# Performance work log

Measured on AMD Instinct MI355X. Metric: run time of the kernel, lower is better.

The kernel has to match this reference:

```python
import jax, jax.numpy as jnp
import numpy as np

L = 4          # stack_size
H = 1024       # hidden_size
N = 16         # num_heads
D = H // N     # size_per_head = 64
F = 4096       # filter_size
B = 2
QLEN = 512
MLEN = 512
CLEN = QLEN + MLEN    # 1024
RLEN = CLEN + QLEN    # 1536
NEG_INF = -1e30
LN_EPS = 1e-12


def setup_inputs() -> dict:
    key = jax.random.key(0)
    ks = jax.random.split(key, 24)
    s = 0.02
    inp = {
        'content_stream': jax.random.normal(ks[0], (B, QLEN, H), jnp.float32),
        'content_mask': jnp.zeros((B, 1, QLEN, CLEN), jnp.float32),
        'position_encoding': jax.random.normal(ks[1], (B, RLEN, H), jnp.float32),
        'segment_matrix': jax.random.randint(ks[2], (B, QLEN, CLEN), 0, 2).astype(bool),
        'mems': jax.random.normal(ks[3], (L, B, MLEN, H), jnp.float32),
        # per-layer attention projection weights [L, H, N, D]
        'w_q': jax.random.normal(ks[4], (L, H, N, D), jnp.float32) * s,
        'w_k': jax.random.normal(ks[5], (L, H, N, D), jnp.float32) * s,
        'w_v': jax.random.normal(ks[6], (L, H, N, D), jnp.float32) * s,
        'w_r': jax.random.normal(ks[7], (L, H, N, D), jnp.float32) * s,
        'w_o': jax.random.normal(ks[8], (L, H, N, D), jnp.float32) * s,
        # FFN
        'ffn_w1': jax.random.normal(ks[9], (L, H, F), jnp.float32) * s,
        'ffn_b1': jnp.zeros((L, F), jnp.float32),
        'ffn_w2': jax.random.normal(ks[10], (L, F, H), jnp.float32) * s,
        'ffn_b2': jnp.zeros((L, H), jnp.float32),
        # LayerNorms (post-attn and post-ffn)
        'ln1_gamma': jnp.ones((L, H), jnp.float32),
        'ln1_beta': jnp.zeros((L, H), jnp.float32),
        'ln2_gamma': jnp.ones((L, H), jnp.float32),
        'ln2_beta': jnp.zeros((L, H), jnp.float32),
        # tied biases [N, D] and per-layer segment encoding [L, 2, N, D]
        'content_bias': jax.random.normal(ks[11], (N, D), jnp.float32) * H ** -0.5,
        'position_bias': jax.random.normal(ks[12], (N, D), jnp.float32) * H ** -0.5,
        'segment_bias': jax.random.normal(ks[13], (N, D), jnp.float32) * H ** -0.5,
        'segment_encoding': jax.random.normal(ks[14], (L, 2, N, D), jnp.float32) * H ** -0.5,
    }
    return inp


def _rel_shift(x, klen):
    # x: [b, n, q, r] -> rel-shifted and sliced to [b, n, q, klen]
    b, n, q, r = x.shape
    x = x.reshape(b, n, r, q)[:, :, 1:, :]
    x = x.reshape(b, n, q, r - 1)[:, :, :, :klen]
    return x


def _layernorm(x, gamma, beta):
    mu = jnp.mean(x, axis=-1, keepdims=True)
    var = jnp.mean(jnp.square(x - mu), axis=-1, keepdims=True)
    return (x - mu) * jax.lax.rsqrt(var + LN_EPS) * gamma + beta


def _forward(content_stream, content_mask, position_encoding, segment_matrix,
             mems, w_q, w_k, w_v, w_r, w_o, ffn_w1, ffn_b1, ffn_w2, ffn_b2,
             ln1_gamma, ln1_beta, ln2_gamma, ln2_beta,
             content_bias, position_bias, segment_bias, segment_encoding):
    x = content_stream
    seg = segment_matrix[:, None, :, :]  # [b,1,q,c]
    for l in range(L):
        context = jnp.concatenate([mems[l], x], axis=1)  # [b,c,h]
        q = jnp.einsum('bih,hnd->bind', x, w_q[l])
        k = jnp.einsum('bjh,hnd->bjnd', context, w_k[l])
        v = jnp.einsum('bjh,hnd->bjnd', context, w_v[l])
        r = jnp.einsum('brh,hnd->brnd', position_encoding, w_r[l])
        # content term
        ac = jnp.einsum('bind,bjnd->bnij', q + content_bias, k)
        # position term with rel-shift trick
        bd = jnp.einsum('bind,brnd->bnir', q + position_bias, r)
        bd = _rel_shift(bd, CLEN)
        # segment term: s in {0: different, 1: same-ish binary indicator}
        ef2 = jnp.einsum('bind,snd->bnis', q + segment_bias, segment_encoding[l])
        ef = jnp.where(seg, ef2[..., 1:2], ef2[..., 0:1])  # [b,n,q,c]
        scores = (ac + bd + ef) * (D ** -0.5)
        scores = scores + content_mask * NEG_INF  # mask==1 -> blocked
        probs = jax.nn.softmax(scores, axis=-1)
        attn = jnp.einsum('bnij,bjnd->bind', probs, v)
        attn_out = jnp.einsum('bind,hnd->bih', attn, w_o[l])
        # post-LN residual blocks (dropout is identity at inference)
        y = _layernorm(attn_out + x, ln1_gamma[l], ln1_beta[l])
        ffn = jnp.maximum(y @ ffn_w1[l] + ffn_b1[l], 0.0) @ ffn_w2[l] + ffn_b2[l]
        x = _layernorm(ffn + y, ln2_gamma[l], ln2_beta[l])
    return x


def reference(content_stream, content_mask, position_encoding, segment_matrix,
              mems, w_q, w_k, w_v, w_r, w_o, ffn_w1, ffn_b1, ffn_w2, ffn_b2,
              ln1_gamma, ln1_beta, ln2_gamma, ln2_beta,
              content_bias, position_bias, segment_bias, segment_encoding):
    return _forward(content_stream, content_mask, position_encoding,
                    segment_matrix, mems, w_q, w_k, w_v, w_r, w_o,
                    ffn_w1, ffn_b1, ffn_w2, ffn_b2,
                    ln1_gamma, ln1_beta, ln2_gamma, ln2_beta,
                    content_bias, position_bias, segment_bias, segment_encoding)
```

## Files before the change

### kernel.cpp

```cpp
#include <hip/hip_runtime.h>
#include <hip/hip_bf16.h>


#define BQ 2
#define QL 512
#define ML 512
#define CL 1024
#define RL 1536
#define HD 1024
#define NH 16
#define DH 64
#define FF 4096
#define NLAYER 4

typedef const float* FP;
typedef const __hip_bfloat16* BP;
typedef unsigned short u16;
typedef __attribute__((ext_vector_type(8))) __bf16 bf16x8;
typedef __attribute__((ext_vector_type(4))) float f32x4;

static __device__ __forceinline__ float b2f(__hip_bfloat16 x) { return __bfloat162float(x); }
static __device__ __forceinline__ u16 f2u(float f) {
    union { __hip_bfloat16 h; u16 u; } c; c.h = __float2bfloat16(f); return c.u;
}
static __device__ __forceinline__ float u2f(u16 u) {
    union { float f; unsigned int i; } c; c.i = ((unsigned int)u) << 16; return c.f;
}

static __device__ __forceinline__ void gll16(const u16* g, u16* l) {
    __builtin_amdgcn_global_load_lds(
        (__attribute__((address_space(1))) void*)(u16*)g,
        (__attribute__((address_space(3))) void*)l, 16, 0, 0);
}

__global__ void sniff_kernel(const unsigned int* __restrict__ ln1_gamma,
                             const unsigned char* __restrict__ seg,
                             int* __restrict__ flags) {
    if (threadIdx.x == 0) {
        flags[0] = (ln1_gamma[0] == 0x3F800000u) ? 1 : 0;
        int int32ok = 1;
        for (int i = 0; i < 256; ++i)
            if ((i & 3) != 0 && seg[i] != 0) { int32ok = 0; break; }
        flags[1] = int32ok;
    }
}

__global__ void canon_kernel(FP inf, BP inb, u16* __restrict__ out,
                             int n, const int* __restrict__ flags) {
    int i = blockIdx.x * 256 + threadIdx.x;
    if (i >= n) return;
    out[i] = flags[0] ? f2u(inf[i]) : ((const u16*)inb)[i];
}

__global__ void out_write_kernel(const u16* __restrict__ in, void* __restrict__ out,
                                 int n, const int* __restrict__ flags) {
    int i = blockIdx.x * 256 + threadIdx.x;
    if (i >= n) return;
    if (flags[0]) ((float*)out)[i] = u2f(in[i]);
    else          ((u16*)out)[i] = in[i];
}

__global__ void segmask_pack_kernel(const void* __restrict__ seg,
                                    FP maskf, BP maskb,
                                    unsigned char* __restrict__ segp,
                                    u16* __restrict__ maskS,
                                    const int* __restrict__ flags) {
    int i = blockIdx.x * 256 + threadIdx.x;
    if (i >= BQ * QL * CL) return;
    int sv = flags[1] ? ((const int*)seg)[i] : (int)((const signed char*)seg)[i];
    segp[i] = sv ? 1 : 0;
    float mk = flags[0] ? maskf[i] : b2f(maskb[i]);
    maskS[i] = f2u(mk * -1e30f);
}

__global__ __launch_bounds__(256) void transpose_kernel(
    FP inf, BP inb, u16* __restrict__ out, int R, int Cc,
    const int* __restrict__ flags) {
    __shared__ float t[32][33];
    const int tid = threadIdx.x;
    const int c0 = blockIdx.x * 32, r0 = blockIdx.y * 32;
    const int tc = tid & 31, tr = tid >> 5;
    const int f32 = flags[0];
    #pragma unroll
    for (int p = 0; p < 4; ++p) {
        int r = r0 + p * 8 + tr;
        size_t gi = (size_t)r * Cc + c0 + tc;
        t[p * 8 + tr][tc] = f32 ? inf[gi] : b2f(inb[gi]);
    }
    __syncthreads();
    #pragma unroll
    for (int p = 0; p < 4; ++p) {
        int c = c0 + p * 8 + tr;
        out[(size_t)c * R + r0 + tc] = f2u(t[tc][p * 8 + tr]);
    }
}

__global__ __launch_bounds__(256) void vtrans_kernel(
    const u16* __restrict__ Vb, u16* __restrict__ VT) {
    __shared__ u16 t[32][33];
    const int tid = threadIdx.x;
    const int j0 = blockIdx.x * 32, d0 = blockIdx.y * 32, bn = blockIdx.z;
    const int b = bn >> 4, n = bn & 15;
    const int tc = tid & 31, tr = tid >> 5;
    #pragma unroll
    for (int p = 0; p < 4; ++p) {
        int j = j0 + p * 8 + tr;
        t[p * 8 + tr][tc] = Vb[((size_t)(b * CL + j) * NH + n) * DH + d0 + tc];
    }
    __syncthreads();
    #pragma unroll
    for (int p = 0; p < 4; ++p) {
        int d = d0 + p * 8 + tr;
        VT[((size_t)bn * DH + d) * CL + j0 + tc] = t[tc][p * 8 + tr];
    }
}

__global__ void build_ctx_kernel(FP memf, BP memb, const u16* __restrict__ X,
                                 u16* __restrict__ CTX, const int* __restrict__ flags) {
    int i = blockIdx.x * 256 + threadIdx.x;
    int h = i % HD;
    int r = (i / HD) % CL;
    int b = i / (HD * CL);
    if (r < ML) {
        size_t mi = ((size_t)(b * ML + r)) * HD + h;
        CTX[i] = flags[0] ? f2u(memf[mi]) : ((const u16*)memb)[mi];
    } else {
        CTX[i] = X[((size_t)(b * QL + (r - ML))) * HD + h];
    }
}

__device__ __forceinline__ void gemm128_core(
    const u16* __restrict__ A, int lda, const u16* __restrict__ Bt, int ldb,
    int K, int tid, u16* sA, u16* sB, f32x4 (&acc)[4][4])
{
    const int lane = tid & 63, w = tid >> 6;
    const int wm = (w & 1) * 64, wn = (w >> 1) * 64;
    const int lr = lane & 15, quad = lane >> 4;
    const int srow = lane >> 2;
    const int sch = (lane & 3) * 8;

    for (int k0 = 0; k0 < K; k0 += 32) {
        #pragma unroll
        for (int j = 0; j < 2; ++j) {
            int rb = w * 32 + j * 16;
            gll16(&A[(size_t)(rb + srow) * lda + k0 + sch], &sA[rb * 32 + lane * 8]);
            gll16(&Bt[(size_t)(rb + srow) * ldb + k0 + sch], &sB[rb * 32 + lane * 8]);
        }
        __syncthreads();
        bf16x8 af[4], bf[4];
        #pragma unroll
        for (int mi = 0; mi < 4; ++mi)
            af[mi] = *(const bf16x8*)&sA[(wm + mi * 16 + lr) * 32 + quad * 8];
        #pragma unroll
        for (int ni = 0; ni < 4; ++ni)
            bf[ni] = *(const bf16x8*)&sB[(wn + ni * 16 + lr) * 32 + quad * 8];
        #pragma unroll
        for (int mi = 0; mi < 4; ++mi)
            #pragma unroll
            for (int ni = 0; ni < 4; ++ni)
                acc[mi][ni] = __builtin_amdgcn_mfma_f32_16x16x32_bf16(
                    af[mi], bf[ni], acc[mi][ni], 0, 0, 0);
        __syncthreads();
    }
}

#define ACC_INIT(acc) \
    _Pragma("unroll") for (int mi = 0; mi < 4; ++mi) \
        _Pragma("unroll") for (int ni = 0; ni < 4; ++ni) \
            acc[mi][ni] = (f32x4){0.f, 0.f, 0.f, 0.f};

__global__ __launch_bounds__(256) void proj4_gemm(
    const u16* __restrict__ X, const u16* __restrict__ CTX,
    const u16* __restrict__ PE, const u16* __restrict__ W4,
    u16* __restrict__ Qb, u16* __restrict__ Kb,
    u16* __restrict__ Vb, u16* __restrict__ Rb)
{
    __shared__ __align__(16) u16 sA[128 * 32];
    __shared__ __align__(16) u16 sB[128 * 32];
    const int tid = threadIdx.x;
    const int by = blockIdx.y;
    const u16* Abase; u16* Cbase; int seg, mb;
    if (by < 8)       { seg = 0; Abase = X;   Cbase = Qb; mb = by; }
    else if (by < 24) { seg = 1; Abase = CTX; Cbase = Kb; mb = by - 8; }
    else if (by < 40) { seg = 2; Abase = CTX; Cbase = Vb; mb = by - 24; }
    else              { seg = 3; Abase = PE;  Cbase = Rb; mb = by - 40; }
    const int m0 = mb * 128, n0 = blockIdx.x * 128;

    f32x4 acc[4][4];
    ACC_INIT(acc)
    gemm128_core(Abase + (size_t)m0 * HD, HD,
                 W4 + (size_t)seg * HD * HD + (size_t)n0 * HD, HD, HD,
                 tid, sA, sB, acc);

    const int lane = tid & 63, w = tid >> 6;
    const int wm = (w & 1) * 64, wn = (w >> 1) * 64;
    const int lr = lane & 15, quad = lane >> 4;
    #pragma unroll
    for (int ni = 0; ni < 4; ++ni) {
        int col = n0 + wn + ni * 16 + lr;
        #pragma unroll
        for (int mi = 0; mi < 4; ++mi) {
            int row = m0 + wm + mi * 16 + quad * 4;
            #pragma unroll
            for (int r = 0; r < 4; ++r)
                Cbase[(size_t)(row + r) * HD + col] = f2u(acc[mi][ni][r]);
        }
    }
}

template <bool RELU, bool HASBIAS>
__global__ __launch_bounds__(256) void mfma_gemm128(
    const u16* __restrict__ A, const u16* __restrict__ Bt,
    FP biasf, BP biasb, u16* __restrict__ C,
    int N, int K, const int* __restrict__ flags)
{
    __shared__ __align__(16) u16 sA[128 * 32];
    __shared__ __align__(16) u16 sB[128 * 32];
    const int tid = threadIdx.x;
    const int n0 = blockIdx.x * 128, m0 = blockIdx.y * 128;
    f32x4 acc[4][4];
    ACC_INIT(acc)
    gemm128_core(A + (size_t)m0 * K, K, Bt + (size_t)n0 * K, K, K,
                 tid, sA, sB, acc);

    const int lane = tid & 63, w = tid >> 6;
    const int wm = (w & 1) * 64, wn = (w >> 1) * 64;
    const int lr = lane & 15, quad = lane >> 4;
    const int f32 = flags[0];
    #pragma unroll
    for (int ni = 0; ni < 4; ++ni) {
        int col = n0 + wn + ni * 16 + lr;
        float bv = 0.f;
        if (HASBIAS) bv = f32 ? biasf[col] : b2f(biasb[col]);
        #pragma unroll
        for (int mi = 0; mi < 4; ++mi) {
            int row = m0 + wm + mi * 16 + quad * 4;
            #pragma unroll
            for (int r = 0; r < 4; ++r) {
                float v = acc[mi][ni][r];
                if (HASBIAS) v += bv;
                if (RELU) v = fmaxf(v, 0.0f);
                C[(size_t)(row + r) * N + col] = f2u(v);
            }
        }
    }
}

__global__ __launch_bounds__(256) void gemm128_splitk(
    const u16* __restrict__ A, const u16* __restrict__ Bt,
    float* __restrict__ part, int N, int Kfull, int Kc)
{
    __shared__ __align__(16) u16 sA[128 * 32];
    __shared__ __align__(16) u16 sB[128 * 32];
    const int tid = threadIdx.x;
    const int n0 = blockIdx.x * 128, m0 = blockIdx.y * 128, z = blockIdx.z;
    f32x4 acc[4][4];
    ACC_INIT(acc)
    gemm128_core(A + (size_t)m0 * Kfull + z * Kc, Kfull,
                 Bt + (size_t)n0 * Kfull + z * Kc, Kfull, Kc,
                 tid, sA, sB, acc);

    float* P = part + (size_t)z * (1024 * 1024);
    const int lane = tid & 63, w = tid >> 6;
    const int wm = (w & 1) * 64, wn = (w >> 1) * 64;
    const int lr = lane & 15, quad = lane >> 4;
    #pragma unroll
    for (int ni = 0; ni < 4; ++ni) {
        int col = n0 + wn + ni * 16 + lr;
        #pragma unroll
        for (int mi = 0; mi < 4; ++mi) {
            int row = m0 + wm + mi * 16 + quad * 4;
            #pragma unroll
            for (int r = 0; r < 4; ++r)
                P[(size_t)(row + r) * N + col] = acc[mi][ni][r];
        }
    }
}

template <bool HASBIAS>
__global__ __launch_bounds__(256) void reduce_add_ln(
    const float* __restrict__ part, FP biasf, BP biasb,
    const u16* __restrict__ resid, FP gf, BP gb, FP bef, BP beb,
    u16* __restrict__ O, const int* __restrict__ flags)
{
    const int row = blockIdx.x;
    const int tid = threadIdx.x;
    const int wid = tid >> 6, lane = tid & 63;
    __shared__ float r1[4], r2[4];
    const int f32 = flags[0];
    float v[4];
    #pragma unroll
    for (int c = 0; c < 4; ++c) {
        int h = c * 256 + tid;
        size_t idx = (size_t)row * HD + h;
        float s = part[idx] + part[idx + 1048576] + part[idx + 2097152] + part[idx + 3145728];
        if (HASBIAS) s += f32 ? biasf[h] : b2f(biasb[h]);
        v[c] = s + u2f(resid[idx]);
    }
    float s = v[0] + v[1] + v[2] + v[3];
    #pragma unroll
    for (int o = 32; o > 0; o >>= 1) s += __shfl_xor(s, o);
    if (lane == 0) r1[wid] = s;
    __syncthreads();
    float mu = (r1[0] + r1[1] + r1[2] + r1[3]) * (1.0f / HD);
    float q = 0.f;
    #pragma unroll
    for (int c = 0; c < 4; ++c) { float d = v[c] - mu; q += d * d; }
    #pragma unroll
    for (int o = 32; o > 0; o >>= 1) q += __shfl_xor(q, o);
    if (lane == 0) r2[wid] = q;
    __syncthreads();
    float var = (r2[0] + r2[1] + r2[2] + r2[3]) * (1.0f / HD);
    float inv = rsqrtf(var + 1e-12f);
    #pragma unroll
    for (int c = 0; c < 4; ++c) {
        int h = c * 256 + tid;
        float g = f32 ? gf[h] : b2f(gb[h]);
        float be = f32 ? bef[h] : b2f(beb[h]);
        O[(size_t)row * HD + h] = f2u((v[c] - mu) * inv * g + be);
    }
}

__global__ void ef2_kernel(const u16* __restrict__ Qb, FP sbf, BP sbb,
                           FP sef, BP seb, float* __restrict__ EF,
                           const int* __restrict__ flags) {
    int t = blockIdx.x * 256 + threadIdx.x;
    if (t >= BQ * NH * QL) return;
    int i = t % QL;
    int n = (t / QL) % NH;
    int b = t / (QL * NH);
    float e0 = 0.f, e1 = 0.f;
    const int f32 = flags[0];
    for (int d = 0; d < DH; ++d) {
        float sbv = f32 ? sbf[n * DH + d] : b2f(sbb[n * DH + d]);
        float s0 = f32 ? sef[(0 * NH + n) * DH + d] : b2f(seb[(0 * NH + n) * DH + d]);
        float s1 = f32 ? sef[(1 * NH + n) * DH + d] : b2f(seb[(1 * NH + n) * DH + d]);
        float qv = u2f(Qb[((size_t)(b * QL + i) * NH + n) * DH + d]) + sbv;
        e0 += qv * s0;
        e1 += qv * s1;
    }
    EF[(size_t)t * 2 + 0] = e0;
    EF[(size_t)t * 2 + 1] = e1;
}

__global__ void ckpr_kernel(const u16* __restrict__ Kb, const u16* __restrict__ Rb,
                            FP cbf, BP cbb, FP pbf, BP pbb,
                            float* __restrict__ CK, float* __restrict__ PR,
                            const int* __restrict__ flags) {
    int t = blockIdx.x * 256 + threadIdx.x;
    const int f32 = flags[0];
    if (t < 32 * CL) {
        int bn = t >> 10, j = t & (CL - 1);
        int b = bn >> 4, n = bn & 15;
        float s = 0.f;
        for (int d = 0; d < DH; ++d) {
            float c = f32 ? cbf[n * DH + d] : b2f(cbb[n * DH + d]);
            s += c * u2f(Kb[((size_t)(b * CL + j) * NH + n) * DH + d]);
        }
        CK[t] = s;
    } else {
        int t2 = t - 32 * CL;
        if (t2 >= 32 * RL) return;
        int bn = t2 / RL, rr = t2 % RL;
        int b = bn >> 4, n = bn & 15;
        float s = 0.f;
        for (int d = 0; d < DH; ++d) {
            float c = f32 ? pbf[n * DH + d] : b2f(pbb[n * DH + d]);
            s += c * u2f(Rb[((size_t)(b * RL + rr) * NH + n) * DH + d]);
        }
        PR[(size_t)bn * RL + rr] = s;
    }
}

#define FA_SP 72
#define FA_SD 84
__global__ __launch_bounds__(128) void flash_attn_kernel(
    const u16* __restrict__ Qb, const u16* __restrict__ Kb,
    const u16* __restrict__ Rb, const u16* __restrict__ VT,
    const float* __restrict__ CK, const float* __restrict__ PR,
    const float* __restrict__ EF, const unsigned char* __restrict__ segp,
    const u16* __restrict__ maskS, u16* __restrict__ AT)
{
    __shared__ __align__(16) u16 sP[2][16 * FA_SP];
    __shared__ float sD[2][16 * FA_SD];
    __shared__ float cmb[64 * 25];

    const int tid = threadIdx.x;
    const int w = tid >> 6;
    const int lane = tid & 63;
    const int lr = lane & 15, quad = lane >> 4;

    const int blin = blockIdx.x;
    const int xcd = blin & 7, slot = blin >> 3;
    const int bn = xcd + 8 * (slot >> 5);
    const int itile = slot & 31;
    const int b = bn >> 4, n = bn & 15;
    const int i0 = itile * 16;

    u16* myP = sP[w];
    float* myD = sD[w];

    const size_t qoff = ((size_t)(b * QL + i0 + lr) * NH + n) * DH + quad * 8;
    const bf16x8 q0 = *(const bf16x8*)&Qb[qoff];
    const bf16x8 q1 = *(const bf16x8*)&Qb[qoff + 32];

    float ef0[4], ef1[4];
    #pragma unroll
    for (int r = 0; r < 4; ++r) {
        size_t e = ((size_t)bn * QL + i0 + quad * 4 + r) * 2;
        ef0[r] = EF[e]; ef1[r] = EF[e + 1];
    }

    f32x4 accO[4];
    #pragma unroll
    for (int c = 0; c < 4; ++c) accO[c] = (f32x4){0.f, 0.f, 0.f, 0.f};
    float m[4], l[4];
    #pragma unroll
    for (int r = 0; r < 4; ++r) { m[r] = -1e38f; l[r] = 0.f; }

    for (int t = 0; t < 8; ++t) {
        const int j0 = (2 * t + w) * 64;
        const int base16 = 497 - i0 + j0;

        f32x4 acc[4];
        #pragma unroll
        for (int c = 0; c < 4; ++c) acc[c] = (f32x4){0.f, 0.f, 0.f, 0.f};
        #pragma unroll
        for (int ct = 0; ct < 4; ++ct) {
            const u16* kp = &Kb[((size_t)(b * CL + j0 + ct * 16 + lr) * NH + n) * DH + quad * 8];
            acc[ct] = __builtin_amdgcn_mfma_f32_16x16x32_bf16(q0, *(const bf16x8*)kp, acc[ct], 0, 0, 0);
            acc[ct] = __builtin_amdgcn_mfma_f32_16x16x32_bf16(q1, *(const bf16x8*)(kp + 32), acc[ct], 0, 0, 0);
        }
        f32x4 bd[5];
        int rrl[5];
        #pragma unroll
        for (int f = 0; f < 5; ++f) {
            bd[f] = (f32x4){0.f, 0.f, 0.f, 0.f};
            int rr = base16 + f * 16 + lr;
            rr = rr > RL - 1 ? RL - 1 : rr;
            rrl[f] = rr;
            const u16* rp = &Rb[((size_t)(b * RL + rr) * NH + n) * DH + quad * 8];
            bd[f] = __builtin_amdgcn_mfma_f32_16x16x32_bf16(q0, *(const bf16x8*)rp, bd[f], 0, 0, 0);
            bd[f] = __builtin_amdgcn_mfma_f32_16x16x32_bf16(q1, *(const bf16x8*)(rp + 32), bd[f], 0, 0, 0);
        }
        #pragma unroll
        for (int f = 0; f < 5; ++f) {
            float prv = PR[(size_t)bn * RL + rrl[f]];
            #pragma unroll
            for (int r = 0; r < 4; ++r)
                myD[(quad * 4 + r) * FA_SD + f * 16 + lr] = bd[f][r] + prv;
        }
        #pragma unroll
        for (int ct = 0; ct < 4; ++ct) {
            float ckv = CK[(size_t)bn * CL + j0 + ct * 16 + lr];
            #pragma unroll
            for (int r = 0; r < 4; ++r) {
                int ilw = quad * 4 + r;
                int p = 15 - ilw + ct * 16 + lr;
                float bdv = myD[ilw * FA_SD + p];
                size_t mi = ((size_t)(b * QL + i0 + ilw)) * CL + j0 + ct * 16 + lr;
                float efv = segp[mi] ? ef1[r] : ef0[r];
                acc[ct][r] = (acc[ct][r] + bdv + ckv + efv) * 0.125f + u2f(maskS[mi]);
            }
        }
        float a[4];
        #pragma unroll
        for (int r = 0; r < 4; ++r) {
            float tm = fmaxf(fmaxf(acc[0][r], acc[1][r]), fmaxf(acc[2][r], acc[3][r]));
            tm = fmaxf(tm, __shfl_xor(tm, 1));
            tm = fmaxf(tm, __shfl_xor(tm, 2));
            tm = fmaxf(tm, __shfl_xor(tm, 4));
            tm = fmaxf(tm, __shfl_xor(tm, 8));
            float mn = fmaxf(m[r], tm);
            a[r] = __expf(m[r] - mn);
            m[r] = mn;
        }
        float ts[4] = {0.f, 0.f, 0.f, 0.f};
        #pragma unroll
        for (int ct = 0; ct < 4; ++ct)
            #pragma unroll
            for (int r = 0; r < 4; ++r) {
                float pv = __expf(acc[ct][r] - m[r]);
                ts[r] += pv;
                myP[(quad * 4 + r) * FA_SP + ct * 16 + lr] = f2u(pv);
            }
        #pragma unroll
        for (int r = 0; r < 4; ++r) {
            float s = ts[r];
            s += __shfl_xor(s, 1);
            s += __shfl_xor(s, 2);
            s += __shfl_xor(s, 4);
            s += __shfl_xor(s, 8);
            l[r] = l[r] * a[r] + s;
            #pragma unroll
            for (int c = 0; c < 4; ++c) accO[c][r] *= a[r];
        }
        const bf16x8 pa0 = *(const bf16x8*)&myP[lr * FA_SP + quad * 8];
        const bf16x8 pa1 = *(const bf16x8*)&myP[lr * FA_SP + 32 + quad * 8];
        #pragma unroll
        for (int ct = 0; ct < 4; ++ct) {
            const u16* vp = &VT[((size_t)bn * DH + ct * 16 + lr) * CL + j0 + quad * 8];
            accO[ct] = __builtin_amdgcn_mfma_f32_16x16x32_bf16(pa0, *(const bf16x8*)vp, accO[ct], 0, 0, 0);
            accO[ct] = __builtin_amdgcn_mfma_f32_16x16x32_bf16(pa1, *(const bf16x8*)(vp + 32), accO[ct], 0, 0, 0);
        }
    }
    if (w == 1) {
        float* c = &cmb[lane * 25];
        #pragma unroll
        for (int ct = 0; ct < 4; ++ct)
            #pragma unroll
            for (int r = 0; r < 4; ++r) c[ct * 4 + r] = accO[ct][r];
        #pragma unroll
        for (int r = 0; r < 4; ++r) { c[16 + r] = m[r]; c[20 + r] = l[r]; }
    }
    __syncthreads();
    if (w == 0) {
        const float* c = &cmb[lane * 25];
        float e0[4], e1[4], inv[4];
        #pragma unroll
        for (int r = 0; r < 4; ++r) {
            float m1 = c[16 + r], l1 = c[20 + r];
            float M = fmaxf(m[r], m1);
            e0[r] = __expf(m[r] - M);
            e1[r] = __expf(m1 - M);
            inv[r] = 1.0f / (l[r] * e0[r] + l1 * e1[r]);
        }
        #pragma unroll
        for (int ct = 0; ct < 4; ++ct)
            #pragma unroll
            for (int r = 0; r < 4; ++r) {
                float o = accO[ct][r] * e0[r] + c[ct * 4 + r] * e1[r];
                AT[((size_t)(b * QL + i0 + quad * 4 + r) * NH + n) * DH + ct * 16 + lr]
                    = f2u(o * inv[r]);
            }
    }
}

extern "C" void kernel_launch(void* const* d_in, const int* in_sizes, int n_in,
                              void* d_out, int out_size, void* d_ws, size_t ws_size,
                              hipStream_t stream) {
    (void)in_sizes; (void)n_in; (void)out_size; (void)ws_size;
    const void* content_stream = d_in[0];
    const void* content_mask   = d_in[1];
    const void* pos_enc        = d_in[2];
    const void* seg_mat        = d_in[3];
    const void* mems           = d_in[4];
    const void* w_q            = d_in[5];
    const void* w_k            = d_in[6];
    const void* w_v            = d_in[7];
    const void* w_r            = d_in[8];
    const void* w_o            = d_in[9];
    const void* ffn_w1         = d_in[10];
    const void* ffn_b1         = d_in[11];
    const void* ffn_w2         = d_in[12];
    const void* ffn_b2         = d_in[13];
    const void* ln1_g          = d_in[14];
    const void* ln1_b          = d_in[15];
    const void* ln2_g          = d_in[16];
    const void* ln2_b          = d_in[17];
    const void* cb             = d_in[18];
    const void* pb             = d_in[19];
    const void* sb             = d_in[20];
    const void* se             = d_in[21];

    float* SC    = (float*)d_ws;
    float* PART  = SC + 4194304;
    float* EF    = SC + 16777216;
    float* CK    = EF + 32768;
    float* PR    = CK + 32768;
    int*   flags = (int*)(PR + 49152);
    u16*   bws   = (u16*)(flags + 16);

    u16* X   = bws;               u16* Y   = X   + 1048576;
    u16* CTX = Y   + 1048576;     u16* Qb  = CTX + 2097152;
    u16* Kb  = Qb  + 1048576;     u16* Vb  = Kb  + 2097152;
    u16* Rb  = Vb  + 2097152;     u16* PE  = Rb  + 3145728;
    u16* AT  = PE  + 3145728;
    u16* W4  = AT  + 1048576;
    u16* WOc = W4  + 4194304;     u16* W1T = WOc + 1048576;
    u16* W2T = W1T + 4194304;
    u16* F1  = (u16*)SC;
    u16* VT  = (u16*)(SC + 8388608);
    unsigned char* segp = (unsigned char*)(SC + 9437184);
    u16* maskS = (u16*)(SC + 9699328);

    const size_t wstride   = (size_t)HD * HD;
    const size_t memstride = (size_t)BQ * ML * HD;

    const dim3 blk(256);
    #define DUAL(base, off) ((FP)(base) + (off)), ((BP)(base) + (off))

    sniff_kernel<<<dim3(1), dim3(64), 0, stream>>>(
        (const unsigned int*)ln1_g, (const unsigned char*)seg_mat, flags);

    canon_kernel<<<dim3((BQ * QL * HD) / 256), blk, 0, stream>>>(
        DUAL(content_stream, 0), X, BQ * QL * HD, flags);
    canon_kernel<<<dim3((BQ * RL * HD) / 256), blk, 0, stream>>>(
        DUAL(pos_enc, 0), PE, BQ * RL * HD, flags);
    segmask_pack_kernel<<<dim3((BQ * QL * CL) / 256), blk, 0, stream>>>(
        seg_mat, DUAL(content_mask, 0), segp, maskS, flags);

    for (int l = 0; l < NLAYER; ++l) {
        transpose_kernel<<<dim3(32, 32), blk, 0, stream>>>(
            DUAL(w_q, (size_t)l * wstride), W4, HD, HD, flags);
        transpose_kernel<<<dim3(32, 32), blk, 0, stream>>>(
            DUAL(w_k, (size_t)l * wstride), W4 + 1048576, HD, HD, flags);
        transpose_kernel<<<dim3(32, 32), blk, 0, stream>>>(
            DUAL(w_v, (size_t)l * wstride), W4 + 2097152, HD, HD, flags);
        transpose_kernel<<<dim3(32, 32), blk, 0, stream>>>(
            DUAL(w_r, (size_t)l * wstride), W4 + 3145728, HD, HD, flags);
        canon_kernel<<<dim3((HD * HD) / 256), blk, 0, stream>>>(
            DUAL(w_o, (size_t)l * wstride), WOc, HD * HD, flags);
        transpose_kernel<<<dim3(FF / 32, HD / 32), blk, 0, stream>>>(
            DUAL(ffn_w1, (size_t)l * HD * FF), W1T, HD, FF, flags);
        transpose_kernel<<<dim3(HD / 32, FF / 32), blk, 0, stream>>>(
            DUAL(ffn_w2, (size_t)l * FF * HD), W2T, FF, HD, flags);

        build_ctx_kernel<<<dim3((BQ * CL * HD) / 256), blk, 0, stream>>>(
            DUAL(mems, (size_t)l * memstride), X, CTX, flags);

        proj4_gemm<<<dim3(8, 64), blk, 0, stream>>>(
            X, CTX, PE, W4, Qb, Kb, Vb, Rb);

        ef2_kernel<<<dim3((BQ * NH * QL) / 256), blk, 0, stream>>>(
            Qb, DUAL(sb, 0), DUAL(se, (size_t)l * 2 * NH * DH), EF, flags);
        ckpr_kernel<<<dim3((32 * CL + 32 * RL) / 256), blk, 0, stream>>>(
            Kb, Rb, DUAL(cb, 0), DUAL(pb, 0), CK, PR, flags);
        vtrans_kernel<<<dim3(CL / 32, DH / 32, BQ * NH), blk, 0, stream>>>(Vb, VT);

        flash_attn_kernel<<<dim3(1024), dim3(128), 0, stream>>>(
            Qb, Kb, Rb, VT, CK, PR, EF, segp, maskS, AT);

        gemm128_splitk<<<dim3(8, 8, 4), blk, 0, stream>>>(
            AT, WOc, PART, HD, HD, 256);
        reduce_add_ln<false><<<dim3(BQ * QL), blk, 0, stream>>>(
            PART, (FP)nullptr, (BP)nullptr, X,
            DUAL(ln1_g, (size_t)l * HD), DUAL(ln1_b, (size_t)l * HD), Y, flags);

        mfma_gemm128<true, true><<<dim3(FF / 128, (BQ * QL) / 128), blk, 0, stream>>>(
            Y, W1T, DUAL(ffn_b1, (size_t)l * FF), F1, FF, HD, flags);

        gemm128_splitk<<<dim3(8, 8, 4), blk, 0, stream>>>(
            F1, W2T, PART, HD, FF, 1024);
        reduce_add_ln<true><<<dim3(BQ * QL), blk, 0, stream>>>(
            PART, DUAL(ffn_b2, (size_t)l * HD), Y,
            DUAL(ln2_g, (size_t)l * HD), DUAL(ln2_b, (size_t)l * HD), X, flags);
    }
    #undef DUAL

    out_write_kernel<<<dim3((BQ * QL * HD) / 256), blk, 0, stream>>>(
        X, d_out, BQ * QL * HD, flags);
}
```

Baseline: 1.374 ms.

## Split attention KV across four waves, prefetch tiles, pack segment bit into mask

The flash attention kernel now uses four waves per block, each covering a quarter of the key range, and merges their partial softmax states at the end through shared memory reused from the score scratch buffer. All K, R, V, PR, CK and mask loads for a tile are issued up front, before the MFMAs, to expose memory-level parallelism. The separate segment byte array is dropped: the segment bit is packed into the LSB of the bf16 mask value, which removes one global read per score element. This costs more registers per thread and a four-way final combine, and it perturbs the mask value's low bit.

```diff
diff --git a/kernel.cpp b/kernel.cpp
--- a/kernel.cpp
+++ b/kernel.cpp
@@ -62,15 +62,13 @@
 
 __global__ void segmask_pack_kernel(const void* __restrict__ seg,
                                     FP maskf, BP maskb,
-                                    unsigned char* __restrict__ segp,
                                     u16* __restrict__ maskS,
                                     const int* __restrict__ flags) {
     int i = blockIdx.x * 256 + threadIdx.x;
     if (i >= BQ * QL * CL) return;
     int sv = flags[1] ? ((const int*)seg)[i] : (int)((const signed char*)seg)[i];
-    segp[i] = sv ? 1 : 0;
     float mk = flags[0] ? maskf[i] : b2f(maskb[i]);
-    maskS[i] = f2u(mk * -1e30f);
+    maskS[i] = (u16)((f2u(mk * -1e30f) & 0xFFFEu) | (sv ? 1u : 0u));
 }
 
 __global__ __launch_bounds__(256) void transpose_kernel(
@@ -374,16 +372,15 @@
 
 #define FA_SP 72
 #define FA_SD 84
-__global__ __launch_bounds__(128) void flash_attn_kernel(
+__global__ __launch_bounds__(256, 4) void flash_attn_kernel(
     const u16* __restrict__ Qb, const u16* __restrict__ Kb,
     const u16* __restrict__ Rb, const u16* __restrict__ VT,
     const float* __restrict__ CK, const float* __restrict__ PR,
-    const float* __restrict__ EF, const unsigned char* __restrict__ segp,
+    const float* __restrict__ EF,
     const u16* __restrict__ maskS, u16* __restrict__ AT)
 {
-    __shared__ __align__(16) u16 sP[2][16 * FA_SP];
-    __shared__ float sD[2][16 * FA_SD];
-    __shared__ float cmb[64 * 25];
+    __shared__ __align__(16) u16 sP[4][16 * FA_SP];
+    __shared__ __align__(16) float sD[4][16 * FA_SD];
 
     const int tid = threadIdx.x;
     const int w = tid >> 6;
@@ -418,49 +415,79 @@
     #pragma unroll
     for (int r = 0; r < 4; ++r) { m[r] = -1e38f; l[r] = 0.f; }
 
-    for (int t = 0; t < 8; ++t) {
-        const int j0 = (2 * t + w) * 64;
+    #pragma unroll
+    for (int t = 0; t < 4; ++t) {
+        const int j0 = (4 * t + w) * 64;
         const int base16 = 497 - i0 + j0;
 
+        bf16x8 kf[8];
+        const u16* kbase = &Kb[((size_t)(b * CL + j0 + lr) * NH + n) * DH + quad * 8];
+        #pragma unroll
+        for (int ct = 0; ct < 4; ++ct) {
+            const u16* kp = kbase + (size_t)ct * 16 * (NH * DH);
+            kf[ct * 2]     = *(const bf16x8*)kp;
+            kf[ct * 2 + 1] = *(const bf16x8*)(kp + 32);
+        }
+        bf16x8 rf[10]; float prv[5];
+        #pragma unroll
+        for (int f = 0; f < 5; ++f) {
+            int rr = base16 + f * 16 + lr;
+            rr = rr > RL - 1 ? RL - 1 : rr;
+            const u16* rp = &Rb[((size_t)(b * RL + rr) * NH + n) * DH + quad * 8];
+            rf[f * 2]     = *(const bf16x8*)rp;
+            rf[f * 2 + 1] = *(const bf16x8*)(rp + 32);
+            prv[f] = PR[(size_t)bn * RL + rr];
+        }
+        float ckv[4];
+        u16 msv[4][4];
+        #pragma unroll
+        for (int ct = 0; ct < 4; ++ct) {
+            ckv[ct] = CK[(size_t)bn * CL + j0 + ct * 16 + lr];
+            #pragma unroll
+            for (int r = 0; r < 4; ++r) {
+                size_t mi = ((size_t)(b * QL + i0 + quad * 4 + r)) * CL + j0 + ct * 16 + lr;
+                msv[ct][r] = maskS[mi];
+            }
+        }
+        bf16x8 vf[8];
+        #pragma unroll
+        for (int ct = 0; ct < 4; ++ct) {
+            const u16* vp = &VT[((size_t)bn * DH + ct * 16 + lr) * CL + j0 + quad * 8];
+            vf[ct * 2]     = *(const bf16x8*)vp;
+            vf[ct * 2 + 1] = *(const bf16x8*)(vp + 32);
+        }
+
         f32x4 acc[4];
         #pragma unroll
         for (int c = 0; c < 4; ++c) acc[c] = (f32x4){0.f, 0.f, 0.f, 0.f};
         #pragma unroll
         for (int ct = 0; ct < 4; ++ct) {
-            const u16* kp = &Kb[((size_t)(b * CL + j0 + ct * 16 + lr) * NH + n) * DH + quad * 8];
-            acc[ct] = __builtin_amdgcn_mfma_f32_16x16x32_bf16(q0, *(const bf16x8*)kp, acc[ct], 0, 0, 0);
-            acc[ct] = __builtin_amdgcn_mfma_f32_16x16x32_bf16(q1, *(const bf16x8*)(kp + 32), acc[ct], 0, 0, 0);
+            acc[ct] = __builtin_amdgcn_mfma_f32_16x16x32_bf16(q0, kf[ct * 2], acc[ct], 0, 0, 0);
+            acc[ct] = __builtin_amdgcn_mfma_f32_16x16x32_bf16(q1, kf[ct * 2 + 1], acc[ct], 0, 0, 0);
         }
         f32x4 bd[5];
-        int rrl[5];
         #pragma unroll
         for (int f = 0; f < 5; ++f) {
             bd[f] = (f32x4){0.f, 0.f, 0.f, 0.f};
-            int rr = base16 + f * 16 + lr;
-            rr = rr > RL - 1 ? RL - 1 : rr;
-            rrl[f] = rr;
-            const u16* rp = &Rb[((size_t)(b * RL + rr) * NH + n) * DH + quad * 8];
-            bd[f] = __builtin_amdgcn_mfma_f32_16x16x32_bf16(q0, *(const bf16x8*)rp, bd[f], 0, 0, 0);
-            bd[f] = __builtin_amdgcn_mfma_f32_16x16x32_bf16(q1, *(const bf16x8*)(rp + 32), bd[f], 0, 0, 0);
-        }
-        #pragma unroll
-        for (int f = 0; f < 5; ++f) {
-            float prv = PR[(size_t)bn * RL + rrl[f]];
+            bd[f] = __builtin_amdgcn_mfma_f32_16x16x32_bf16(q0, rf[f * 2], bd[f], 0, 0, 0);
+            bd[f] = __builtin_amdgcn_mfma_f32_16x16x32_bf16(q1, rf[f * 2 + 1], bd[f], 0, 0, 0);
+        }
+        #pragma unroll
+        for (int f = 0; f < 5; ++f)
             #pragma unroll
             for (int r = 0; r < 4; ++r)
-                myD[(quad * 4 + r) * FA_SD + f * 16 + lr] = bd[f][r] + prv;
-        }
+                myD[(quad * 4 + r) * FA_SD + f * 16 + lr] = bd[f][r] + prv[f];
         #pragma unroll
         for (int ct = 0; ct < 4; ++ct) {
-            float ckv = CK[(size_t)bn * CL + j0 + ct * 16 + lr];
             #pragma unroll
             for (int r = 0; r < 4; ++r) {
                 int ilw = quad * 4 + r;
                 int p = 15 - ilw + ct * 16 + lr;
                 float bdv = myD[ilw * FA_SD + p];
-                size_t mi = ((size_t)(b * QL + i0 + ilw)) * CL + j0 + ct * 16 + lr;
-                float efv = segp[mi] ? ef1[r] : ef0[r];
-                acc[ct][r] = (acc[ct][r] + bdv + ckv + efv) * 0.125f + u2f(maskS[mi]);
+                u16 mv = msv[ct][r];
+                float efv = (mv & 1) ? ef1[r] : ef0[r];
+                float mka = u2f((u16)(mv & 0xFFFEu));
+                acc[ct][r] = (acc[ct][r] + bdv + ckv[ct] + efv) * 0.125f + mka;
             }
         }
         float a[4];
@@ -499,13 +526,14 @@
         const bf16x8 pa1 = *(const bf16x8*)&myP[lr * FA_SP + 32 + quad * 8];
         #pragma unroll
         for (int ct = 0; ct < 4; ++ct) {
-            const u16* vp = &VT[((size_t)bn * DH + ct * 16 + lr) * CL + j0 + quad * 8];
-            accO[ct] = __builtin_amdgcn_mfma_f32_16x16x32_bf16(pa0, *(const bf16x8*)vp, accO[ct], 0, 0, 0);
-            accO[ct] = __builtin_amdgcn_mfma_f32_16x16x32_bf16(pa1, *(const bf16x8*)(vp + 32), accO[ct], 0, 0, 0);
-        }
-    }
-    if (w == 1) {
-        float* c = &cmb[lane * 25];
+            accO[ct] = __builtin_amdgcn_mfma_f32_16x16x32_bf16(pa0, vf[ct * 2], accO[ct], 0, 0, 0);
+            accO[ct] = __builtin_amdgcn_mfma_f32_16x16x32_bf16(pa1, vf[ct * 2 + 1], accO[ct], 0, 0, 0);
+        }
+    }
+    __syncthreads();
+    float* cmb = &sD[0][0];
+    if (w != 0) {
+        float* c = &cmb[((w - 1) * 64 + lane) * 25];
         #pragma unroll
         for (int ct = 0; ct < 4; ++ct)
             #pragma unroll
@@ -515,23 +543,36 @@
     }
     __syncthreads();
     if (w == 0) {
-        const float* c = &cmb[lane * 25];
-        float e0[4], e1[4], inv[4];
-        #pragma unroll
-        for (int r = 0; r < 4; ++r) {
-            float m1 = c[16 + r], l1 = c[20 + r];
-            float M = fmaxf(m[r], m1);
-            e0[r] = __expf(m[r] - M);
-            e1[r] = __expf(m1 - M);
-            inv[r] = 1.0f / (l[r] * e0[r] + l1 * e1[r]);
+        float M[4], es[4], eo[3][4], lt[4];
+        #pragma unroll
+        for (int r = 0; r < 4; ++r) M[r] = m[r];
+        #pragma unroll
+        for (int k = 0; k < 3; ++k) {
+            const float* c = &cmb[(k * 64 + lane) * 25];
+            #pragma unroll
+            for (int r = 0; r < 4; ++r) M[r] = fmaxf(M[r], c[16 + r]);
+        }
+        #pragma unroll
+        for (int r = 0; r < 4; ++r) { es[r] = __expf(m[r] - M[r]); lt[r] = l[r] * es[r]; }
+        #pragma unroll
+        for (int k = 0; k < 3; ++k) {
+            const float* c = &cmb[(k * 64 + lane) * 25];
+            #pragma unroll
+            for (int r = 0; r < 4; ++r) {
+                eo[k][r] = __expf(c[16 + r] - M[r]);
+                lt[r] += c[20 + r] * eo[k][r];
+            }
         }
         #pragma unroll
         for (int ct = 0; ct < 4; ++ct)
             #pragma unroll
             for (int r = 0; r < 4; ++r) {
-                float o = accO[ct][r] * e0[r] + c[ct * 4 + r] * e1[r];
+                float o = accO[ct][r] * es[r];
+                #pragma unroll
+                for (int k = 0; k < 3; ++k)
+                    o += cmb[(k * 64 + lane) * 25 + ct * 4 + r] * eo[k][r];
                 AT[((size_t)(b * QL + i0 + quad * 4 + r) * NH + n) * DH + ct * 16 + lr]
-                    = f2u(o * inv[r]);
+                    = f2u(o / lt[r]);
             }
     }
 }
@@ -581,7 +622,6 @@
     u16* W2T = W1T + 4194304;
     u16* F1  = (u16*)SC;
     u16* VT  = (u16*)(SC + 8388608);
-    unsigned char* segp = (unsigned char*)(SC + 9437184);
     u16* maskS = (u16*)(SC + 9699328);
 
     const size_t wstride   = (size_t)HD * HD;
@@ -598,7 +638,7 @@
     canon_kernel<<<dim3((BQ * RL * HD) / 256), blk, 0, stream>>>(
         DUAL(pos_enc, 0), PE, BQ * RL * HD, flags);
     segmask_pack_kernel<<<dim3((BQ * QL * CL) / 256), blk, 0, stream>>>(
-        seg_mat, DUAL(content_mask, 0), segp, maskS, flags);
+        seg_mat, DUAL(content_mask, 0), maskS, flags);
 
     for (int l = 0; l < NLAYER; ++l) {
         transpose_kernel<<<dim3(32, 32), blk, 0, stream>>>(
@@ -628,8 +668,8 @@
             Kb, Rb, DUAL(cb, 0), DUAL(pb, 0), CK, PR, flags);
         vtrans_kernel<<<dim3(CL / 32, DH / 32, BQ * NH), blk, 0, stream>>>(Vb, VT);
 
-        flash_attn_kernel<<<dim3(1024), dim3(128), 0, stream>>>(
-            Qb, Kb, Rb, VT, CK, PR, EF, segp, maskS, AT);
+        flash_attn_kernel<<<dim3(1024), dim3(256), 0, stream>>>(
+            Qb, Kb, Rb, VT, CK, PR, EF, maskS, AT);
 
         gemm128_splitk<<<dim3(8, 8, 4), blk, 0, stream>>>(
             AT, WOc, PART, HD, HD, 256);
```

New measurement: 1.362 ms. No clear change (-0.9%).
